# Kernel tuning notes

Measured on AMD Instinct MI355X. Metric: run time of the kernel, lower is better.

The kernel has to match this reference:

```python
import jax, jax.numpy as jnp
import numpy as np

HEADS = 8
HEAD_DIM = 32
SCALE = HEAD_DIM ** (-0.5)


def setup_inputs() -> dict:
    key = jax.random.key(0)
    k1, k2, k3 = jax.random.split(key, 3)
    B, DIM, N = 4, 512, 2048
    INNER = HEADS * HEAD_DIM  # 256
    x = jax.random.normal(k1, (B, DIM, N), dtype=jnp.float32)
    # Conv1d(kernel=1, bias=False) == channel-mixing matmul; weight (out_ch, in_ch)
    w_qkv = jax.random.normal(k2, (3 * INNER, DIM), dtype=jnp.float32) * (DIM ** -0.5)
    w_out = jax.random.normal(k3, (DIM, INNER), dtype=jnp.float32) * (INNER ** -0.5)
    b_out = jnp.zeros((DIM,), dtype=jnp.float32)
    return {"x": x, "w_qkv": w_qkv, "w_out": w_out, "b_out": b_out}


def reference(x, w_qkv, w_out, b_out):
    B, DIM, N = x.shape
    INNER = HEADS * HEAD_DIM
    # to_qkv: 1x1 conv over channels, then permute(0,2,1) -> (B, N, 3*INNER)
    qkv = jnp.einsum('bcn,oc->bno', x, w_qkv)
    q, k, v = jnp.split(qkv, 3, axis=-1)
    # 'b n (h d) -> b h n d'
    def to_heads(t):
        return t.reshape(B, N, HEADS, HEAD_DIM).transpose(0, 2, 1, 3)
    q, k, v = to_heads(q), to_heads(k), to_heads(v)
    # L2 similarity: -||q_i - k_j||_2 * scale, via expansion (avoids O(N^2 d) tensor)
    q2 = jnp.sum(q * q, axis=-1)            # (B,H,N)
    k2 = jnp.sum(k * k, axis=-1)            # (B,H,N)
    qk = jnp.einsum('bhid,bhjd->bhij', q, k)  # (B,H,N,N)
    dist2 = q2[..., :, None] + k2[..., None, :] - 2.0 * qk
    smi = -jnp.sqrt(jnp.maximum(dist2, 1e-12)) * SCALE
    attn = jax.nn.softmax(smi, axis=-1)
    out = jnp.einsum('bhij,bhjd->bhid', attn, v)  # (B,H,N,d)
    # 'b h n d -> b (h d) n'
    out = out.transpose(0, 1, 3, 2).reshape(B, INNER, N)
    # to_out: 1x1 conv with bias
    return jnp.einsum('bcn,oc->bon', out, w_out) + b_out[None, :, None]
```

## Files before the change

### kernel.cpp

```cpp
#include <hip/hip_runtime.h>
#include <math.h>

#define N_SEQ 2048
#define DIMC 512
#define INNER 256
#define C2F (0.17677669529663687f * 1.4426950408889634f)
#define C2F2 (C2F * C2F)

typedef short bf16x8 __attribute__((ext_vector_type(8)));
typedef float f32x4 __attribute__((ext_vector_type(4)));


static __device__ __forceinline__ ushort f2bf(float f) {
    uint x = __float_as_uint(f);
    x += 0x7fff + ((x >> 16) & 1);
    return (ushort)(x >> 16);
}
static __device__ __forceinline__ float bf2f(ushort u) {
    return __uint_as_float(((uint)u) << 16);
}
static __device__ __forceinline__ float fast_exp2_neg(float x) {
    float r; asm("v_exp_f32 %0, -%1" : "=v"(r) : "v"(x)); return r;
}
static __device__ __forceinline__ float fast_sqrt(float x) {
    float r; asm("v_sqrt_f32 %0, %1" : "=v"(r) : "v"(x)); return r;
}
static __device__ __forceinline__ void gload16(const void* g, void* l) {
    __builtin_amdgcn_global_load_lds(
        (const __attribute__((address_space(1))) void*)g,
        (__attribute__((address_space(3))) void*)l, 16, 0, 0);
}

__global__ void prep_kernel(const float* __restrict__ x,
                            const float* __restrict__ wq,
                            const float* __restrict__ wo,
                            ushort* __restrict__ xt,
                            ushort* __restrict__ wq16,
                            ushort* __restrict__ wo16) {
    __shared__ __align__(16) ushort T[64][72];
    const int bid = blockIdx.x;
    const int t = threadIdx.x;
    if (bid < 1024) {
        const int n0 = (bid & 31) * 64;
        const int c0 = ((bid >> 5) & 7) * 64;
        const int b = bid >> 8;
        const int cl = t >> 4;
        const int n4 = (t & 15) * 4;
        const float* xb = x + ((size_t)b * DIMC + c0) * N_SEQ + n0;
#pragma unroll
        for (int cc = 0; cc < 4; ++cc) {
            const int c = cl + cc * 16;
            float4 v = *(const float4*)(xb + (size_t)c * N_SEQ + n4);
            T[n4 + 0][c] = f2bf(v.x);
            T[n4 + 1][c] = f2bf(v.y);
            T[n4 + 2][c] = f2bf(v.z);
            T[n4 + 3][c] = f2bf(v.w);
        }
        __syncthreads();
        const int nl = t >> 2;
        const int c16 = (t & 3) * 16;
        uint4 v0 = *(const uint4*)&T[nl][c16];
        uint4 v1 = *(const uint4*)&T[nl][c16 + 8];
        ushort* dst = xt + ((size_t)b * N_SEQ + n0 + nl) * DIMC + c0 + c16;
        *(uint4*)dst = v0;
        *(uint4*)(dst + 8) = v1;
    } else if (bid < 1408) {
        int i = ((bid - 1024) * 256 + t) * 4;
        float4 v = *(const float4*)(wq + i);
        ushort4 p;
        p.x = f2bf(v.x); p.y = f2bf(v.y); p.z = f2bf(v.z); p.w = f2bf(v.w);
        *(ushort4*)(wq16 + i) = p;
    } else {
        int i = ((bid - 1408) * 256 + t) * 4;
        float4 v = *(const float4*)(wo + i);
        ushort4 p;
        p.x = f2bf(v.x); p.y = f2bf(v.y); p.z = f2bf(v.z); p.w = f2bf(v.w);
        *(ushort4*)(wo16 + i) = p;
    }
}

__global__ __launch_bounds__(256) void qkv_mfma(const ushort* __restrict__ xt,
        const ushort* __restrict__ w16, ushort* __restrict__ ws16) {
    __shared__ __align__(16) ushort Wls[4 * 520];
    __shared__ __align__(16) ushort Xls[4 * 520];
    const int b = blockIdx.z;
    const int o0 = blockIdx.y * 64;
    const int n0 = blockIdx.x * 64;
    const int t = threadIdx.x;
    const int l = t & 63, w = t >> 6;
    const int q15 = l & 15, g = l >> 4;
    f32x4 acc[4];
#pragma unroll
    for (int nn = 0; nn < 4; ++nn) acc[nn] = (f32x4){0.f, 0.f, 0.f, 0.f};
    const int srow = t >> 2, sg = t & 3;
    const ushort* wsrc = w16 + (size_t)(o0 + srow) * DIMC + sg * 8;
    const ushort* xsrc = xt + ((size_t)b * N_SEQ + n0 + srow) * DIMC + sg * 8;
    uint4 wreg = *(const uint4*)wsrc;
    uint4 xreg = *(const uint4*)xsrc;
    for (int k0 = 0; k0 < DIMC; k0 += 32) {
        __builtin_amdgcn_s_barrier();
        __builtin_amdgcn_sched_barrier(0);
        *(uint4*)(Wls + sg * 520 + srow * 8) = wreg;
        *(uint4*)(Xls + sg * 520 + srow * 8) = xreg;
        if (k0 + 32 < DIMC) {
            wreg = *(const uint4*)(wsrc + k0 + 32);
            xreg = *(const uint4*)(xsrc + k0 + 32);
        }
        asm volatile("s_waitcnt lgkmcnt(0)" ::: "memory");
        __builtin_amdgcn_s_barrier();
        __builtin_amdgcn_sched_barrier(0);
        bf16x8 af = *(const bf16x8*)(Wls + g * 520 + (16 * w + q15) * 8);
        __builtin_amdgcn_s_setprio(1);
#pragma unroll
        for (int nn = 0; nn < 4; ++nn) {
            bf16x8 bfr = *(const bf16x8*)(Xls + g * 520 + (16 * nn + q15) * 8);
            acc[nn] = __builtin_amdgcn_mfma_f32_16x16x32_bf16(af, bfr, acc[nn], 0, 0, 0);
        }
        __builtin_amdgcn_s_setprio(0);
    }
    const int oatom = o0 + 16 * w;
    const int t_idx = oatom >> 8;
    const int h = (oatom >> 5) & 7;
    const int bh = b * 8 + h;
    const int d0 = (oatom & 31) + 4 * g;
    if (t_idx < 2) {
        ushort* dst = ws16 + (size_t)t_idx * 2097152 + (size_t)bh * 65536
                      + (size_t)(d0 >> 3) * 16384 + (d0 & 7);
#pragma unroll
        for (int nn = 0; nn < 4; ++nn) {
            const int n_ = n0 + 16 * nn + q15;
            ushort4 p;
            p.x = f2bf(acc[nn][0]); p.y = f2bf(acc[nn][1]);
            p.z = f2bf(acc[nn][2]); p.w = f2bf(acc[nn][3]);
            *(ushort4*)(dst + (size_t)n_ * 8) = p;
        }
    } else {
        ushort* dst = ws16 + (size_t)4194304 + (size_t)bh * 65536;
#pragma unroll
        for (int nn = 0; nn < 4; ++nn) {
            const int n_ = n0 + 16 * nn + q15;
            ushort* dd = dst + (size_t)(n_ >> 3) * 256 + (n_ & 7);
            dd[(d0 + 0) * 8] = f2bf(acc[nn][0]);
            dd[(d0 + 1) * 8] = f2bf(acc[nn][1]);
            dd[(d0 + 2) * 8] = f2bf(acc[nn][2]);
            dd[(d0 + 3) * 8] = f2bf(acc[nn][3]);
        }
    }
}

__global__ void sq_kernel(const ushort* __restrict__ ws16, float* __restrict__ k2) {
    const int idx = blockIdx.x * 256 + threadIdx.x;
    const int bh = idx >> 11, n = idx & 2047;
    const ushort* base = ws16 + 2097152 + (size_t)bh * 65536 + (size_t)n * 8;
    float s = 0.f;
#pragma unroll
    for (int g = 0; g < 4; ++g) {
        uint4 v = *(const uint4*)(base + (size_t)g * 16384);
        uint a[4] = {v.x, v.y, v.z, v.w};
#pragma unroll
        for (int e = 0; e < 4; ++e) {
            float lo = bf2f((ushort)(a[e] & 0xffff));
            float hi = bf2f((ushort)(a[e] >> 16));
            s += lo * lo + hi * hi;
        }
    }
    k2[idx] = s * (float)C2F2;
}

__global__ __launch_bounds__(256, 4) void attn_kernel(
        const ushort* __restrict__ ws16, const float* __restrict__ k2g,
        ushort* __restrict__ att16) {
    __shared__ __align__(16) ushort Kls[2 * 2048];
    __shared__ __align__(16) ushort Vls[2 * 2048];
    __shared__ __align__(16) float k2ls[2048];
    __shared__ __align__(16) ushort Pls[4][16][72];
    const int bid = blockIdx.x;
    const int sw = (bid & 7) * 128 + (bid >> 3);
    const int q0 = (sw & 31) * 64;
    const int bh = sw >> 5;
    const int b = bh >> 3, h = bh & 7;
    const int tid = threadIdx.x;
    const int l = tid & 63;
    const int w = tid >> 6;
    const int q15 = l & 15;
    const int g = l >> 4;
    const int qrow = q0 + 16 * w + q15;

    const ushort* Qbh = ws16 + (size_t)bh * 65536;
    const ushort* Kbh = ws16 + 2097152 + (size_t)bh * 65536;
    const ushort* Vbh = ws16 + 4194304 + (size_t)bh * 65536;
    const float* k2bh = k2g + (size_t)bh * 2048;

#define STAGE(T, BUF)                                                         \
    {                                                                         \
        const int j0s = (T) * 64;                                             \
        gload16(Kbh + (size_t)w * 16384 + (size_t)(j0s + l) * 8,              \
                Kls + (BUF) * 2048 + w * 512);                                \
        gload16(Vbh + (size_t)j0s * 32 + (size_t)w * 512 + (size_t)l * 8,     \
                Vls + (BUF) * 2048 + w * 512);                                \
    }

    gload16(k2bh + (size_t)(2 * w + 0) * 256 + (size_t)l * 4, k2ls + (2 * w + 0) * 256);
    gload16(k2bh + (size_t)(2 * w + 1) * 256 + (size_t)l * 4, k2ls + (2 * w + 1) * 256);
    STAGE(0, 0)

    const bf16x8 qf = *(const bf16x8*)(Qbh + (size_t)g * 16384 + (size_t)qrow * 8);
    float q2l = 0.f;
#pragma unroll
    for (int e = 0; e < 8; ++e) {
        float qe = bf2f((ushort)qf[e]);
        q2l = fmaf(qe, qe, q2l);
    }
    q2l += __shfl_xor(q2l, 16);
    q2l += __shfl_xor(q2l, 32);
    const float q2v = q2l * (float)C2F2;

    ushort* plane = &Pls[w][q15][0];
    f32x4 accO[2];
    accO[0] = (f32x4){0.f, 0.f, 0.f, 0.f};
    accO[1] = (f32x4){0.f, 0.f, 0.f, 0.f};
    float lsm = 0.f;

    asm volatile("s_waitcnt vmcnt(0)" ::: "memory");
    __builtin_amdgcn_s_barrier();
    __builtin_amdgcn_sched_barrier(0);

#define COMPUTE(T)                                                              \
    {                                                                           \
        const ushort* KlsP = Kls + ((T) & 1) * 2048;                            \
        const ushort* VlsP = Vls + ((T) & 1) * 2048;                            \
        const int jb = (T) * 64;                                                \
        bf16x8 kf[4];                                                           \
        _Pragma("unroll")                                                       \
        for (int k = 0; k < 4; ++k)                                             \
            kf[k] = *(const bf16x8*)(KlsP + g * 512 + (16 * k + q15) * 8);      \
        const f32x4 zz = (f32x4){0.f, 0.f, 0.f, 0.f};                           \
        f32x4 st[4];                                                            \
        __builtin_amdgcn_s_setprio(1);                                          \
        _Pragma("unroll")                                                       \
        for (int k = 0; k < 4; ++k)                                             \
            st[k] = __builtin_amdgcn_mfma_f32_16x16x32_bf16(kf[k], qf, zz, 0, 0, 0); \
        __builtin_amdgcn_s_setprio(0);                                          \
        float lt = 0.f;                                                         \
        _Pragma("unroll")                                                       \
        for (int k = 0; k < 4; ++k) {                                           \
            float4 kk = *(const float4*)(k2ls + jb + 16 * k + 4 * g);           \
            float ka[4] = {kk.x, kk.y, kk.z, kk.w};                             \
            float pr[4];                                                        \
            _Pragma("unroll")                                                   \
            for (int r = 0; r < 4; ++r) {                                       \
                float a = q2v + ka[r];                                          \
                float d2 = fmaf(-2.f * (float)C2F2, st[k][r], a);               \
                pr[r] = fast_exp2_neg(fast_sqrt(fmaxf(d2, 1e-12f)));            \
            }                                                                   \
            lt += (pr[0] + pr[1]) + (pr[2] + pr[3]);                            \
            uint pk0, pk1;                                                      \
            asm("v_cvt_pk_bf16_f32 %0, %1, %2" : "=v"(pk0) : "v"(pr[0]), "v"(pr[1])); \
            asm("v_cvt_pk_bf16_f32 %0, %1, %2" : "=v"(pk1) : "v"(pr[2]), "v"(pr[3])); \
            uint2 pv; pv.x = pk0; pv.y = pk1;                                   \
            *(uint2*)(plane + 16 * k + 4 * g) = pv;                             \
        }                                                                       \
        lsm += lt;                                                              \
        __builtin_amdgcn_s_setprio(1);                                          \
        _Pragma("unroll")                                                       \
        for (int jc = 0; jc < 2; ++jc) {                                        \
            bf16x8 pf = *(const bf16x8*)(plane + 32 * jc + 8 * g);              \
            _Pragma("unroll")                                                   \
            for (int dh = 0; dh < 2; ++dh) {                                    \
                bf16x8 vf = *(const bf16x8*)(VlsP + (4 * jc + g) * 256          \
                                             + (16 * dh + q15) * 8);            \
                accO[dh] = __builtin_amdgcn_mfma_f32_16x16x32_bf16(vf, pf, accO[dh], 0, 0, 0); \
            }                                                                   \
        }                                                                       \
        __builtin_amdgcn_s_setprio(0);                                          \
    }

#pragma unroll 1
    for (int t = 0; t < 31; ++t) {
        STAGE(t + 1, (t + 1) & 1)
        asm volatile("s_waitcnt vmcnt(2)" ::: "memory");
        __builtin_amdgcn_s_barrier();
        __builtin_amdgcn_sched_barrier(0);
        COMPUTE(t)
        __builtin_amdgcn_sched_barrier(0);
        __builtin_amdgcn_s_barrier();
    }
    asm volatile("s_waitcnt vmcnt(0)" ::: "memory");
    __builtin_amdgcn_s_barrier();
    __builtin_amdgcn_sched_barrier(0);
    COMPUTE(31)
#undef COMPUTE
#undef STAGE

    lsm += __shfl_xor(lsm, 16);
    lsm += __shfl_xor(lsm, 32);
    const float invl = 1.f / lsm;
    ushort* dst = att16 + ((size_t)(b * N_SEQ + qrow)) * INNER + h * 32 + 4 * g;
#pragma unroll
    for (int d = 0; d < 2; ++d) {
        ushort4 o;
        o.x = f2bf(accO[d][0] * invl); o.y = f2bf(accO[d][1] * invl);
        o.z = f2bf(accO[d][2] * invl); o.w = f2bf(accO[d][3] * invl);
        *(ushort4*)(dst + d * 16) = o;
    }
}

__global__ __launch_bounds__(256) void out_mfma(const ushort* __restrict__ att16,
        const ushort* __restrict__ wo16, const float* __restrict__ bias,
        float* __restrict__ out) {
    __shared__ __align__(16) ushort Wls[4 * 520];
    __shared__ __align__(16) ushort Als[4 * 520];
    const int b = blockIdx.z;
    const int o0 = blockIdx.y * 64;
    const int n0 = blockIdx.x * 64;
    const int t = threadIdx.x;
    const int l = t & 63, w = t >> 6;
    const int q15 = l & 15, g = l >> 4;
    f32x4 acc[4];
#pragma unroll
    for (int nn = 0; nn < 4; ++nn) acc[nn] = (f32x4){0.f, 0.f, 0.f, 0.f};
    const int srow = t >> 2, sg = t & 3;
    const ushort* wsrc = wo16 + (size_t)(o0 + srow) * INNER + sg * 8;
    const ushort* asrc = att16 + ((size_t)b * N_SEQ + n0 + srow) * INNER + sg * 8;
    uint4 wreg = *(const uint4*)wsrc;
    uint4 areg = *(const uint4*)asrc;
    for (int k0 = 0; k0 < INNER; k0 += 32) {
        __builtin_amdgcn_s_barrier();
        __builtin_amdgcn_sched_barrier(0);
        *(uint4*)(Wls + sg * 520 + srow * 8) = wreg;
        *(uint4*)(Als + sg * 520 + srow * 8) = areg;
        if (k0 + 32 < INNER) {
            wreg = *(const uint4*)(wsrc + k0 + 32);
            areg = *(const uint4*)(asrc + k0 + 32);
        }
        asm volatile("s_waitcnt lgkmcnt(0)" ::: "memory");
        __builtin_amdgcn_s_barrier();
        __builtin_amdgcn_sched_barrier(0);
        bf16x8 af = *(const bf16x8*)(Wls + g * 520 + (16 * w + q15) * 8);
        __builtin_amdgcn_s_setprio(1);
#pragma unroll
        for (int nn = 0; nn < 4; ++nn) {
            bf16x8 bfr = *(const bf16x8*)(Als + g * 520 + (16 * nn + q15) * 8);
            acc[nn] = __builtin_amdgcn_mfma_f32_16x16x32_bf16(af, bfr, acc[nn], 0, 0, 0);
        }
        __builtin_amdgcn_s_setprio(0);
    }
    const int obase = o0 + 16 * w + 4 * g;
    float4 bi = *(const float4*)(bias + obase);
    float* ob = out + ((size_t)b * DIMC + obase) * N_SEQ;
#pragma unroll
    for (int nn = 0; nn < 4; ++nn) {
        const int n_ = n0 + 16 * nn + q15;
        ob[0 * N_SEQ + n_] = acc[nn][0] + bi.x;
        ob[1 * N_SEQ + n_] = acc[nn][1] + bi.y;
        ob[2 * N_SEQ + n_] = acc[nn][2] + bi.z;
        ob[3 * N_SEQ + n_] = acc[nn][3] + bi.w;
    }
}

extern "C" void kernel_launch(void* const* d_in, const int* in_sizes, int n_in,
                              void* d_out, int out_size, void* d_ws, size_t ws_size,
                              hipStream_t stream) {
    const float* x = (const float*)d_in[0];
    const float* w_qkv = (const float*)d_in[1];
    const float* w_out = (const float*)d_in[2];
    const float* b_out = (const float*)d_in[3];
    ushort* ws16 = (ushort*)d_ws;
    float* k2f = (float*)((char*)d_ws + (12 << 20) + (256 << 10));
    ushort* att16 = (ushort*)((char*)d_ws + (13 << 20));
    ushort* xt16 = (ushort*)((char*)d_ws + (21 << 20));
    ushort* wq16 = (ushort*)((char*)d_ws + (29 << 20));
    ushort* wo16 = (ushort*)((char*)d_ws + (30 << 20));
    float* out = (float*)d_out;

    prep_kernel<<<dim3(1536), 256, 0, stream>>>(x, w_qkv, w_out, xt16, wq16, wo16);
    qkv_mfma<<<dim3(32, 12, 4), 256, 0, stream>>>(xt16, wq16, ws16);
    sq_kernel<<<dim3(256), 256, 0, stream>>>(ws16, k2f);
    attn_kernel<<<dim3(1024), 256, 0, stream>>>(ws16, k2f, att16);
    out_mfma<<<dim3(32, 8, 4), 256, 0, stream>>>(att16, wo16, b_out, out);
}
```

Measured before the change: 86.74 us.

## Triple-buffer K/V/k2 tiles in attention with a single barrier per iteration

Result: no change. 85.81 us (median of 2 runs) (-1.1%).

```diff
diff --git a/kernel.cpp b/kernel.cpp
--- a/kernel.cpp
+++ b/kernel.cpp
@@ -29,6 +29,11 @@
     __builtin_amdgcn_global_load_lds(
         (const __attribute__((address_space(1))) void*)g,
         (__attribute__((address_space(3))) void*)l, 16, 0, 0);
+}
+static __device__ __forceinline__ void gload4(const void* g, void* l) {
+    __builtin_amdgcn_global_load_lds(
+        (const __attribute__((address_space(1))) void*)g,
+        (__attribute__((address_space(3))) void*)l, 4, 0, 0);
 }
 
 __global__ void prep_kernel(const float* __restrict__ x,
@@ -170,9 +175,9 @@
 __global__ __launch_bounds__(256, 4) void attn_kernel(
         const ushort* __restrict__ ws16, const float* __restrict__ k2g,
         ushort* __restrict__ att16) {
-    __shared__ __align__(16) ushort Kls[2 * 2048];
-    __shared__ __align__(16) ushort Vls[2 * 2048];
-    __shared__ __align__(16) float k2ls[2048];
+    __shared__ __align__(16) ushort Kls[3 * 2048];
+    __shared__ __align__(16) ushort Vls[3 * 2048];
+    __shared__ __align__(16) float k2ls[3 * 64];
     __shared__ __align__(16) ushort Pls[4][16][72];
     const int bid = blockIdx.x;
     const int sw = (bid & 7) * 128 + (bid >> 3);
@@ -198,11 +203,11 @@
                 Kls + (BUF) * 2048 + w * 512);                                \
         gload16(Vbh + (size_t)j0s * 32 + (size_t)w * 512 + (size_t)l * 8,     \
                 Vls + (BUF) * 2048 + w * 512);                                \
-    }
-
-    gload16(k2bh + (size_t)(2 * w + 0) * 256 + (size_t)l * 4, k2ls + (2 * w + 0) * 256);
-    gload16(k2bh + (size_t)(2 * w + 1) * 256 + (size_t)l * 4, k2ls + (2 * w + 1) * 256);
+        gload4(k2bh + j0s + l, k2ls + (BUF) * 64);                            \
+    }
+
     STAGE(0, 0)
+    STAGE(1, 1)
 
     const bf16x8 qf = *(const bf16x8*)(Qbh + (size_t)g * 16384 + (size_t)qrow * 8);
     float q2l = 0.f;
@@ -221,15 +226,11 @@
     accO[1] = (f32x4){0.f, 0.f, 0.f, 0.f};
     float lsm = 0.f;
 
-    asm volatile("s_waitcnt vmcnt(0)" ::: "memory");
-    __builtin_amdgcn_s_barrier();
-    __builtin_amdgcn_sched_barrier(0);
-
-#define COMPUTE(T)                                                              \
+#define COMPUTE(BC)                                                             \
     {                                                                           \
-        const ushort* KlsP = Kls + ((T) & 1) * 2048;                            \
-        const ushort* VlsP = Vls + ((T) & 1) * 2048;                            \
-        const int jb = (T) * 64;                                                \
+        const ushort* KlsP = Kls + (BC) * 2048;                                 \
+        const ushort* VlsP = Vls + (BC) * 2048;                                 \
+        const float* k2P = k2ls + (BC) * 64;                                    \
         bf16x8 kf[4];                                                           \
         _Pragma("unroll")                                                       \
         for (int k = 0; k < 4; ++k)                                             \
@@ -244,7 +245,7 @@
         float lt = 0.f;                                                         \
         _Pragma("unroll")                                                       \
         for (int k = 0; k < 4; ++k) {                                           \
-            float4 kk = *(const float4*)(k2ls + jb + 16 * k + 4 * g);           \
+            float4 kk = *(const float4*)(k2P + 16 * k + 4 * g);                 \
             float ka[4] = {kk.x, kk.y, kk.z, kk.w};                             \
             float pr[4];                                                        \
             _Pragma("unroll")                                                   \
@@ -275,20 +276,24 @@
         __builtin_amdgcn_s_setprio(0);                                          \
     }
 
+    int bc = 0;
+    int sb = 2;
 #pragma unroll 1
     for (int t = 0; t < 31; ++t) {
-        STAGE(t + 1, (t + 1) & 1)
-        asm volatile("s_waitcnt vmcnt(2)" ::: "memory");
-        __builtin_amdgcn_s_barrier();
-        __builtin_amdgcn_sched_barrier(0);
-        COMPUTE(t)
-        __builtin_amdgcn_sched_barrier(0);
-        __builtin_amdgcn_s_barrier();
+        asm volatile("s_waitcnt vmcnt(3)" ::: "memory");
+        __builtin_amdgcn_s_barrier();
+        __builtin_amdgcn_sched_barrier(0);
+        COMPUTE(bc)
+        if (t + 2 <= 31) {
+            STAGE(t + 2, sb)
+        }
+        bc = (bc == 2) ? 0 : bc + 1;
+        sb = (sb == 2) ? 0 : sb + 1;
     }
     asm volatile("s_waitcnt vmcnt(0)" ::: "memory");
     __builtin_amdgcn_s_barrier();
     __builtin_amdgcn_sched_barrier(0);
-    COMPUTE(31)
+    COMPUTE(bc)
 #undef COMPUTE
 #undef STAGE
 
```
